# Kernel tuning notes

Measured on AMD Instinct MI355X. Metric: run time of the kernel, lower is better.

## Reference

```python
import jax, jax.numpy as jnp
import numpy as np

B, L, DM, H, DFF = 4, 2048, 512, 8, 2048
D = DM // H            # head dim = 64
FACTOR = 5
U = min(FACTOR * int(np.ceil(np.log(L))), L)  # 40 sampled keys / top-u queries
EPS = 1e-5


def layer_norm(x, g, b):
    m = x.mean(-1, keepdims=True)
    v = ((x - m) ** 2).mean(-1, keepdims=True)
    return (x - m) * jax.lax.rsqrt(v + EPS) * g + b


def setup_inputs() -> dict:
    key = jax.random.key(0)
    ks = jax.random.split(key, 18)
    s = 0.02  # init scale for stability
    return {
        "x": jax.random.normal(ks[0], (B, L, DM), jnp.float32),
        "Wq": jax.random.normal(ks[1], (DM, DM), jnp.float32) * s,
        "bq": jnp.zeros((DM,), jnp.float32),
        "Wk": jax.random.normal(ks[2], (DM, DM), jnp.float32) * s,
        "bk": jnp.zeros((DM,), jnp.float32),
        "Wv": jax.random.normal(ks[3], (DM, DM), jnp.float32) * s,
        "bv": jnp.zeros((DM,), jnp.float32),
        "Wo": jax.random.normal(ks[4], (DM, DM), jnp.float32) * s,
        "bo": jnp.zeros((DM,), jnp.float32),
        "Wc1": jax.random.normal(ks[5], (DFF, DM), jnp.float32) * s,  # conv1d k=1 weight (out,in)
        "bc1": jnp.zeros((DFF,), jnp.float32),
        "Wc2": jax.random.normal(ks[6], (DM, DFF), jnp.float32) * s,
        "bc2": jnp.zeros((DM,), jnp.float32),
        "ln1_g": jnp.ones((DM,), jnp.float32),
        "ln1_b": jnp.zeros((DM,), jnp.float32),
        "ln2_g": jnp.ones((DM,), jnp.float32),
        "ln2_b": jnp.zeros((DM,), jnp.float32),
        "sample_idx": jax.random.randint(ks[7], (L, U), 0, L, jnp.int32),
    }


def reference(x, Wq, bq, Wk, bk, Wv, bv, Wo, bo, Wc1, bc1, Wc2, bc2,
              ln1_g, ln1_b, ln2_g, ln2_b, sample_idx):
    Bb, Ll, _ = x.shape
    # --- AttentionLayer projections -> (B, H, L, D) ---
    q = (x @ Wq + bq).reshape(Bb, Ll, H, D).transpose(0, 2, 1, 3)
    k = (x @ Wk + bk).reshape(Bb, Ll, H, D).transpose(0, 2, 1, 3)
    v = (x @ Wv + bv).reshape(Bb, Ll, H, D).transpose(0, 2, 1, 3)

    # --- ProbSparse: score each query against U sampled keys ---
    K_sample = k[:, :, sample_idx, :]                       # (B,H,L,U,D)
    QK_sample = jnp.einsum('bhld,bhlud->bhlu', q, K_sample)  # (B,H,L,U)
    M = QK_sample.max(-1) - QK_sample.mean(-1)               # sparsity measure (B,H,L)
    _, M_top = jax.lax.top_k(M, U)                           # (B,H,U) top-u query indices

    # --- full attention only for top-u queries ---
    Q_red = jnp.take_along_axis(q, M_top[..., None], axis=2)  # (B,H,U,D)
    scores = jnp.einsum('bhud,bhld->bhul', Q_red, k) / jnp.sqrt(jnp.float32(D))
    attn = jax.nn.softmax(scores, axis=-1)                    # (B,H,U,L)
    ctx_top = jnp.einsum('bhul,bhld->bhud', attn, v)          # (B,H,U,D)

    # --- initial context = mean of V (mask_flag=False); scatter top-u rows ---
    context = jnp.broadcast_to(v.mean(axis=2, keepdims=True), v.shape)
    bi = jnp.arange(Bb)[:, None, None]
    hi = jnp.arange(H)[None, :, None]
    context = context.at[bi, hi, M_top].set(ctx_top)          # (B,H,L,D)

    new_x = context.transpose(0, 2, 1, 3).reshape(Bb, Ll, DM) @ Wo + bo

    # --- residual + norm + conv1d(k=1) FFN + norm ---
    x = layer_norm(x + new_x, ln1_g, ln1_b)
    y = jax.nn.relu(x @ Wc1.T + bc1)
    y = y @ Wc2.T + bc2
    return layer_norm(x + y, ln2_g, ln2_b)
```

## Files before the change

### kernel.cpp

```cpp
#include <hip/hip_runtime.h>
#include <math.h>

static constexpr int Bc = 4, Lc = 2048, DMc = 512, Hc = 8, Dc = 64, DFFc = 2048, Uc = 40;
static constexpr int NT = Bc * Lc;

typedef __attribute__((ext_vector_type(4))) float f32x4;
typedef __attribute__((ext_vector_type(8))) short bf16x8;
typedef unsigned short ushort_t;

__device__ __forceinline__ float wave_sum(float v) {
#pragma unroll
  for (int off = 32; off > 0; off >>= 1) v += __shfl_xor(v, off);
  return v;
}

__device__ __forceinline__ ushort_t f2bf(float f) {
  union { float f; unsigned int u; } c{f};
  unsigned int u = c.u + 0x7fff + ((c.u >> 16) & 1);
  return (ushort_t)(u >> 16);
}

__device__ __forceinline__ float bf2f(ushort_t b) {
  union { unsigned int u; float f; } c{(unsigned int)b << 16};
  return c.f;
}

__device__ __forceinline__ void gload16(const ushort_t* g, ushort_t* l) {
  __builtin_amdgcn_global_load_lds(
      (const __attribute__((address_space(1))) unsigned int*)g,
      (__attribute__((address_space(3))) unsigned int*)l, 16, 0, 0);
}

template <int MODE>
__global__ __launch_bounds__(256) void gemm_mfma(
    const ushort_t* __restrict__ A, const ushort_t* __restrict__ Bt,
    const float* __restrict__ bias, float* __restrict__ Cf,
    ushort_t* __restrict__ Cb, ushort_t* __restrict__ Qo, ushort_t* __restrict__ Ko,
    ushort_t* __restrict__ Vo, int M, int N, int K) {
  __shared__ __align__(16) ushort_t As[128 * 32];
  __shared__ __align__(16) ushort_t Bs[128 * 32];
  const int tid = threadIdx.x;
  const int lane = tid & 63, wave = tid >> 6;
  const int nwg = gridDim.x * gridDim.y;
  const int lin = blockIdx.y * gridDim.x + blockIdx.x;
  const int swz = (lin & 7) * (nwg >> 3) + (lin >> 3);
  const int m0 = (swz / gridDim.x) << 7, n0 = (swz % gridDim.x) << 7;
  const int wm = ((wave >> 1) << 6), wn = ((wave & 1) << 6);
  f32x4 acc[4][4] = {};
  const ushort_t* aSrc = A + (size_t)(m0 + (tid >> 2)) * K + ((tid & 3) << 3);
  const ushort_t* bSrc = Bt + (size_t)(n0 + (tid >> 2)) * K + ((tid & 3) << 3);
  ushort_t* aDst = As + wave * 512;
  ushort_t* bDst = Bs + wave * 512;
  const size_t aHalf = (size_t)64 * K, bHalf = (size_t)64 * K;
  for (int k0 = 0; k0 < K; k0 += 32) {
    gload16(aSrc + k0, aDst);
    gload16(aSrc + aHalf + k0, aDst + 2048);
    gload16(bSrc + k0, bDst);
    gload16(bSrc + bHalf + k0, bDst + 2048);
    __syncthreads();
    bf16x8 af[4], bfr[4];
    const int fr = lane & 15, ko = (lane >> 4) << 3;
#pragma unroll
    for (int i = 0; i < 4; ++i) {
      af[i] = *reinterpret_cast<const bf16x8*>(&As[(wm + i * 16 + fr) * 32 + ko]);
      bfr[i] = *reinterpret_cast<const bf16x8*>(&Bs[(wn + i * 16 + fr) * 32 + ko]);
    }
#pragma unroll
    for (int i = 0; i < 4; ++i)
#pragma unroll
      for (int j = 0; j < 4; ++j)
        acc[i][j] = __builtin_amdgcn_mfma_f32_16x16x32_bf16(af[i], bfr[j], acc[i][j], 0, 0, 0);
    __syncthreads();
  }
  const int cr = (lane >> 4) << 2, cc = lane & 15;
#pragma unroll
  for (int j = 0; j < 4; ++j) {
    const int col = n0 + wn + j * 16 + cc;
    const float bsv = bias[col];
#pragma unroll
    for (int i = 0; i < 4; ++i) {
#pragma unroll
      for (int r = 0; r < 4; ++r) {
        const int row = m0 + wm + i * 16 + cr + r;
        float v = acc[i][j][r] + bsv;
        if (MODE == 0) {
          Cf[(size_t)row * N + col] = v;
        } else if (MODE == 1) {
          Cb[(size_t)row * N + col] = f2bf(fmaxf(v, 0.f));
        } else {
          const int which = col >> 9, h = (col >> 6) & 7, d = col & 63;
          const int b = row >> 11, l = row & (Lc - 1);
          const size_t o = ((size_t)(((b << 3) + h) << 11) + l) * 64 + d;
          ushort_t* dst = which == 0 ? Qo : (which == 1 ? Ko : Vo);
          dst[o] = f2bf(v);
        }
      }
    }
  }
}

__global__ __launch_bounds__(256) void conv_bf16(const float* __restrict__ in,
                                                 ushort_t* __restrict__ out) {
  int i = blockIdx.x * 256 + threadIdx.x;
  float4 v = *reinterpret_cast<const float4*>(&in[(size_t)i * 4]);
  ushort4 o;
  o.x = f2bf(v.x); o.y = f2bf(v.y); o.z = f2bf(v.z); o.w = f2bf(v.w);
  *reinterpret_cast<ushort4*>(&out[(size_t)i * 4]) = o;
}

__global__ __launch_bounds__(256) void tconv(const float* __restrict__ in,
                                             ushort_t* __restrict__ out,
                                             int R, int C, int rowOff) {
  __shared__ float t[32][33];
  const int r0 = blockIdx.y << 5, c0 = blockIdx.x << 5;
  const int tr = threadIdx.x >> 5, tc = threadIdx.x & 31;
#pragma unroll
  for (int p = 0; p < 4; ++p)
    t[tr + p * 8][tc] = in[(size_t)(r0 + tr + p * 8) * C + c0 + tc];
  __syncthreads();
#pragma unroll
  for (int p = 0; p < 4; ++p)
    out[(size_t)(rowOff + c0 + tr + p * 8) * R + r0 + tc] = f2bf(t[tc][tr + p * 8]);
}

__global__ __launch_bounds__(256) void concat_bias(const float* __restrict__ bq,
                                                   const float* __restrict__ bk,
                                                   const float* __restrict__ bv,
                                                   float* __restrict__ o) {
  int i = blockIdx.x * 256 + threadIdx.x;
  o[i] = i < 512 ? bq[i] : (i < 1024 ? bk[i - 512] : bv[i - 1024]);
}

__global__ __launch_bounds__(256) void compute_M_kernel(
    const ushort_t* __restrict__ Q, const ushort_t* __restrict__ K,
    const int* __restrict__ sidx, float* __restrict__ Mout) {
  const int tid = threadIdx.x;
  const int wave = tid >> 6, lane = tid & 63;
  const int g = lane >> 4, lg = lane & 15;
  const int p = blockIdx.x;
  const int xcd = p & 7, j = p >> 3;
  const int bh = xcd + ((j >> 7) << 3);
  const int inner = j & 127;
  const int gw = (bh << 11) + (inner << 4) + wave * 4 + g;
  const int l = gw & (Lc - 1);
  const ushort4 q4 = *reinterpret_cast<const ushort4*>(&Q[((size_t)gw << 6) + (lg << 2)]);
  const float qx = bf2f(q4.x), qy = bf2f(q4.y), qz = bf2f(q4.z), qw = bf2f(q4.w);
  const ushort_t* Kbase = K + ((size_t)bh << 17);
  const int* sp = sidx + l * Uc;
  float mx = -1e30f, sm = 0.f;
#pragma unroll 4
  for (int u = 0; u < Uc; ++u) {
    const int idx = sp[u];
    const ushort4 k4 = *reinterpret_cast<const ushort4*>(&Kbase[((size_t)idx << 6) + (lg << 2)]);
    float d = qx * bf2f(k4.x) + qy * bf2f(k4.y) + qz * bf2f(k4.z) + qw * bf2f(k4.w);
#pragma unroll
    for (int off = 8; off > 0; off >>= 1) d += __shfl_xor(d, off);
    mx = fmaxf(mx, d);
    sm += d;
  }
  if (lg == 0) Mout[gw] = mx - sm * (1.f / Uc);
}

__global__ __launch_bounds__(256) void topk_kernel(const float* __restrict__ Min,
                                                   int* __restrict__ Mtop) {
  __shared__ unsigned sm[Lc];
  __shared__ int scount[4];
  __shared__ int slist[Lc];
  __shared__ int snum;
  const int bh = blockIdx.x;
  const int tid = threadIdx.x;
  const int wv = tid >> 6, lane = tid & 63;
  unsigned sv[8];
#pragma unroll
  for (int t = 0; t < 8; ++t) {
    const unsigned u = __float_as_uint(Min[bh * Lc + tid + (t << 8)]);
    const unsigned s = (u & 0x80000000u) ? ~u : (u | 0x80000000u);
    sv[t] = s;
    sm[tid + (t << 8)] = s;
  }
  if (tid == 0) snum = 0;
  __syncthreads();
  unsigned lo = 0u, hi = 0xFFFFFFFFu;
  while (lo < hi) {
    const unsigned mid =
        (unsigned)(((unsigned long long)lo + (unsigned long long)hi + 1ull) >> 1);
    int cnt = 0;
#pragma unroll
    for (int t = 0; t < 8; ++t) cnt += (sv[t] >= mid);
#pragma unroll
    for (int off = 32; off > 0; off >>= 1) cnt += __shfl_xor(cnt, off);
    if (lane == 0) scount[wv] = cnt;
    __syncthreads();
    const int total = scount[0] + scount[1] + scount[2] + scount[3];
    __syncthreads();
    if (total >= Uc) lo = mid; else hi = mid - 1;
  }
#pragma unroll
  for (int t = 0; t < 8; ++t)
    if (sv[t] >= lo) {
      const int pos = atomicAdd(&snum, 1);
      slist[pos] = tid + (t << 8);
    }
  __syncthreads();
  const int S = snum;
  const int jbase = lane << 5;
  for (int s = wv; s < S; s += 4) {
    const int c = slist[s];
    const unsigned mv = sm[c];
    int rank = 0;
#pragma unroll
    for (int q = 0; q < 8; ++q) {
      const int j = jbase + (q << 2);
      const uint4 w4 = *reinterpret_cast<const uint4*>(&sm[j]);
      rank += (w4.x > mv || (w4.x == mv && (j + 0) < c));
      rank += (w4.y > mv || (w4.y == mv && (j + 1) < c));
      rank += (w4.z > mv || (w4.z == mv && (j + 2) < c));
      rank += (w4.w > mv || (w4.w == mv && (j + 3) < c));
    }
#pragma unroll
    for (int off = 32; off > 0; off >>= 1) rank += __shfl_xor(rank, off);
    if (lane == 0 && rank < Uc) Mtop[bh * Uc + rank] = c;
  }
}

__global__ __launch_bounds__(256, 3) void attn_flash(
    const ushort_t* __restrict__ Q, const ushort_t* __restrict__ K,
    const ushort_t* __restrict__ V, const int* __restrict__ Mtop,
    float* __restrict__ m_p, float* __restrict__ l_p, float* __restrict__ o_p) {
  __shared__ __align__(16) ushort_t Qs[48 * 80];
  __shared__ __align__(16) ushort_t KVs[128 * 80];
  __shared__ __align__(16) ushort_t Ps[48 * 144];
  __shared__ float mw[4][48];
  __shared__ float lw[4][48];
  const int tid = threadIdx.x;
  const int lane = tid & 63, w = tid >> 6;
  const int cc = lane & 15, hi = lane >> 4;
  const int bh = blockIdx.x >> 4, chunk = blockIdx.x & 15;
  const int kk0 = chunk << 7;
  const ushort_t* Qb = Q + ((size_t)bh << 17);
  const ushort_t* Kb = K + ((size_t)bh << 17);
  const ushort_t* Vb = V + ((size_t)bh << 17);

  for (int i = tid; i < 48 * 8; i += 256) {
    const int r = i >> 3, c8 = (i & 7) << 3;
    bf16x8 v = 0;
    if (r < Uc) {
      const int lsel = Mtop[bh * Uc + r];
      v = *reinterpret_cast<const bf16x8*>(&Qb[((size_t)lsel << 6) + c8]);
    }
    *reinterpret_cast<bf16x8*>(&Qs[r * 80 + c8]) = v;
  }
  for (int i = tid; i < 128 * 8; i += 256) {
    const int r = i >> 3, c8 = (i & 7) << 3;
    *reinterpret_cast<bf16x8*>(&KVs[r * 80 + c8]) =
        *reinterpret_cast<const bf16x8*>(&Kb[((size_t)(kk0 + r) << 6) + c8]);
  }
  __syncthreads();

  f32x4 sacc[3][2] = {};
#pragma unroll
  for (int s = 0; s < 2; ++s) {
    bf16x8 af[3], bk[2];
#pragma unroll
    for (int i = 0; i < 3; ++i)
      af[i] = *reinterpret_cast<const bf16x8*>(&Qs[(i * 16 + cc) * 80 + s * 32 + hi * 8]);
#pragma unroll
    for (int jj = 0; jj < 2; ++jj)
      bk[jj] = *reinterpret_cast<const bf16x8*>(&KVs[(w * 32 + jj * 16 + cc) * 80 + s * 32 + hi * 8]);
#pragma unroll
    for (int i = 0; i < 3; ++i)
#pragma unroll
      for (int jj = 0; jj < 2; ++jj)
        sacc[i][jj] = __builtin_amdgcn_mfma_f32_16x16x32_bf16(af[i], bk[jj], sacc[i][jj], 0, 0, 0);
  }

  float mx[3][4];
#pragma unroll
  for (int i = 0; i < 3; ++i)
#pragma unroll
    for (int r = 0; r < 4; ++r)
      mx[i][r] = fmaxf(sacc[i][0][r], sacc[i][1][r]) * 0.125f;
#pragma unroll
  for (int off = 1; off < 16; off <<= 1)
#pragma unroll
    for (int i = 0; i < 3; ++i)
#pragma unroll
      for (int r = 0; r < 4; ++r)
        mx[i][r] = fmaxf(mx[i][r], __shfl_xor(mx[i][r], off));
  if (cc == 0)
#pragma unroll
    for (int i = 0; i < 3; ++i)
#pragma unroll
      for (int r = 0; r < 4; ++r) mw[w][i * 16 + (hi << 2) + r] = mx[i][r];
  __syncthreads();

  float fm[3][4], ls[3][4];
#pragma unroll
  for (int i = 0; i < 3; ++i)
#pragma unroll
    for (int r = 0; r < 4; ++r) {
      const int row = i * 16 + (hi << 2) + r;
      fm[i][r] = fmaxf(fmaxf(mw[0][row], mw[1][row]), fmaxf(mw[2][row], mw[3][row]));
      ls[i][r] = 0.f;
    }
#pragma unroll
  for (int i = 0; i < 3; ++i)
#pragma unroll
    for (int jj = 0; jj < 2; ++jj)
#pragma unroll
      for (int r = 0; r < 4; ++r) {
        float p = __expf(sacc[i][jj][r] * 0.125f - fm[i][r]);
        ls[i][r] += p;
        Ps[(i * 16 + (hi << 2) + r) * 144 + w * 32 + jj * 16 + cc] = f2bf(p);
      }
#pragma unroll
  for (int off = 1; off < 16; off <<= 1)
#pragma unroll
    for (int i = 0; i < 3; ++i)
#pragma unroll
      for (int r = 0; r < 4; ++r) ls[i][r] += __shfl_xor(ls[i][r], off);
  if (cc == 0)
#pragma unroll
    for (int i = 0; i < 3; ++i)
#pragma unroll
      for (int r = 0; r < 4; ++r) lw[w][i * 16 + (hi << 2) + r] = ls[i][r];

  {
    ushort_t* Vt = KVs;
    for (int i = tid; i < 128 * 8; i += 256) {
      const int k = i >> 3, c8 = (i & 7) << 3;
      bf16x8 v = *reinterpret_cast<const bf16x8*>(&Vb[((size_t)(kk0 + k) << 6) + c8]);
#pragma unroll
      for (int jq = 0; jq < 8; ++jq) Vt[(c8 + jq) * 144 + k] = (ushort_t)v[jq];
    }
  }
  __syncthreads();

  f32x4 oacc[3] = {};
#pragma unroll
  for (int s = 0; s < 4; ++s) {
    bf16x8 ap[3], bv;
#pragma unroll
    for (int i = 0; i < 3; ++i)
      ap[i] = *reinterpret_cast<const bf16x8*>(&Ps[(i * 16 + cc) * 144 + s * 32 + hi * 8]);
    bv = *reinterpret_cast<const bf16x8*>(&KVs[(w * 16 + cc) * 144 + s * 32 + hi * 8]);
#pragma unroll
    for (int i = 0; i < 3; ++i)
      oacc[i] = __builtin_amdgcn_mfma_f32_16x16x32_bf16(ap[i], bv, oacc[i], 0, 0, 0);
  }
#pragma unroll
  for (int i = 0; i < 3; ++i)
#pragma unroll
    for (int r = 0; r < 4; ++r) {
      const int row = i * 16 + (hi << 2) + r;
      if (row < Uc)
        o_p[((size_t)((bh * Uc + row) * 16 + chunk) << 6) + w * 16 + cc] = oacc[i][r];
    }
  if (w == 0 && cc == 0)
#pragma unroll
    for (int i = 0; i < 3; ++i)
#pragma unroll
      for (int r = 0; r < 4; ++r) {
        const int row = i * 16 + (hi << 2) + r;
        if (row < Uc) {
          m_p[(bh * Uc + row) * 16 + chunk] = fm[i][r];
          l_p[(bh * Uc + row) * 16 + chunk] =
              lw[0][row] + lw[1][row] + lw[2][row] + lw[3][row];
        }
      }
}

__global__ __launch_bounds__(256) void attn_combine(
    const float* __restrict__ m_p, const float* __restrict__ l_p,
    const float* __restrict__ o_p, const int* __restrict__ Mtop,
    ushort_t* __restrict__ ctxb) {
  const int w = (blockIdx.x * 256 + threadIdx.x) >> 6;
  const int lane = threadIdx.x & 63;
  const float* mp = m_p + w * 16;
  const float* lp = l_p + w * 16;
  float M = -1e30f;
#pragma unroll
  for (int c = 0; c < 16; ++c) M = fmaxf(M, mp[c]);
  float denom = 0.f;
  float wgt[16];
#pragma unroll
  for (int c = 0; c < 16; ++c) {
    wgt[c] = __expf(mp[c] - M);
    denom += lp[c] * wgt[c];
  }
  float acc = 0.f;
#pragma unroll
  for (int c = 0; c < 16; ++c)
    acc += o_p[((size_t)w * 16 + c) * 64 + lane] * wgt[c];
  const int bh = w / Uc;
  const int b = bh >> 3, h = bh & 7;
  const int lsel = Mtop[w];
  ctxb[(size_t)(b * Lc + lsel) * DMc + (h << 6) + lane] = f2bf(acc / denom);
}

__global__ __launch_bounds__(64) void vmean_kernel(const ushort_t* __restrict__ V,
                                                   float* __restrict__ vmean) {
  int blk = blockIdx.x;
  int bh = blk >> 3, c = blk & 7;
  int lane = threadIdx.x;
  float sm = 0.f;
  int lbase = c << 8;
  for (int l = lbase; l < lbase + 256; ++l)
    sm += bf2f(V[((size_t)(bh * Lc + l) << 6) + lane]);
  atomicAdd(&vmean[(bh << 6) + lane], sm * (1.f / Lc));
}

__global__ __launch_bounds__(256) void build_ctx_kernel(const float* __restrict__ vmean,
                                                        ushort_t* __restrict__ ctxb) {
  int idx = blockIdx.x * 256 + threadIdx.x;
  ctxb[idx] = f2bf(vmean[((idx >> 20) << 9) + (idx & 511)]);
}

__global__ __launch_bounds__(256) void add_ln_kernel(
    const float* __restrict__ resid, const float* __restrict__ yin,
    const float* __restrict__ g, const float* __restrict__ bbias,
    float* __restrict__ out, ushort_t* __restrict__ outb) {
  __shared__ float vals[DMc];
  __shared__ float red[4];
  int row = blockIdx.x, tid = threadIdx.x;
  size_t base = (size_t)row * DMc;
  float lsum = 0.f;
  for (int c = tid; c < DMc; c += 256) {
    float t = resid[base + c] + yin[base + c];
    vals[c] = t;
    lsum += t;
  }
  lsum = wave_sum(lsum);
  if ((tid & 63) == 0) red[tid >> 6] = lsum;
  __syncthreads();
  float mean = (red[0] + red[1] + red[2] + red[3]) * (1.f / DMc);
  __syncthreads();
  float lv = 0.f;
  for (int c = tid; c < DMc; c += 256) {
    float dv = vals[c] - mean;
    lv += dv * dv;
  }
  lv = wave_sum(lv);
  if ((tid & 63) == 0) red[tid >> 6] = lv;
  __syncthreads();
  float inv = rsqrtf((red[0] + red[1] + red[2] + red[3]) * (1.f / DMc) + 1e-5f);
  for (int c = tid; c < DMc; c += 256) {
    float o = (vals[c] - mean) * inv * g[c] + bbias[c];
    out[base + c] = o;
    if (outb) outb[base + c] = f2bf(o);
  }
}

extern "C" void kernel_launch(void* const* d_in, const int* in_sizes, int n_in,
                              void* d_out, int out_size, void* d_ws, size_t ws_size,
                              hipStream_t stream) {
  (void)in_sizes; (void)n_in; (void)out_size; (void)ws_size;
  const float* x   = (const float*)d_in[0];
  const float* Wq  = (const float*)d_in[1];
  const float* bq  = (const float*)d_in[2];
  const float* Wk  = (const float*)d_in[3];
  const float* bk  = (const float*)d_in[4];
  const float* Wv  = (const float*)d_in[5];
  const float* bv  = (const float*)d_in[6];
  const float* Wo  = (const float*)d_in[7];
  const float* bo  = (const float*)d_in[8];
  const float* Wc1 = (const float*)d_in[9];
  const float* bc1 = (const float*)d_in[10];
  const float* Wc2 = (const float*)d_in[11];
  const float* bc2 = (const float*)d_in[12];
  const float* g1  = (const float*)d_in[13];
  const float* b1  = (const float*)d_in[14];
  const float* g2  = (const float*)d_in[15];
  const float* b2  = (const float*)d_in[16];
  const int* sidx  = (const int*)d_in[17];
  float* out = (float*)d_out;

  float* ws = (float*)d_ws;
  ushort_t* Qb   = (ushort_t*)ws;
  ushort_t* Kb   = (ushort_t*)(ws + 4194304);
  ushort_t* Vb   = (ushort_t*)(ws + 8388608);
  float* m_p    = ws + 12582912;
  float* l_p    = ws + 12603392;
  float* o_p    = ws + 12623872;
  float* X1     = ws + 16777216;
  ushort_t* xb   = (ushort_t*)(ws + 20971520);
  ushort_t* Wqkvt= (ushort_t*)(ws + 23068672);
  ushort_t* Wot  = (ushort_t*)(ws + 23461888);
  ushort_t* Wc1b = (ushort_t*)(ws + 23592960);
  ushort_t* Wc2b = (ushort_t*)(ws + 24117248);
  float* bqkv   = ws + 24641536;
  float* Mb     = ws + 24643072;
  float* vmean  = ws + 24708608;
  int* Mtop     = (int*)(ws + 24710656);
  ushort_t* CTXb = Vb;
  ushort_t* X1b  = (ushort_t*)(ws + 12582912);
  ushort_t* Yb   = (ushort_t*)ws;

  dim3 blk(256);
  conv_bf16<<<4096, blk, 0, stream>>>(x, xb);
  tconv<<<dim3(16, 16), blk, 0, stream>>>(Wq, Wqkvt, 512, 512, 0);
  tconv<<<dim3(16, 16), blk, 0, stream>>>(Wk, Wqkvt, 512, 512, 512);
  tconv<<<dim3(16, 16), blk, 0, stream>>>(Wv, Wqkvt, 512, 512, 1024);
  tconv<<<dim3(16, 16), blk, 0, stream>>>(Wo, Wot, 512, 512, 0);
  conv_bf16<<<1024, blk, 0, stream>>>(Wc1, Wc1b);
  conv_bf16<<<1024, blk, 0, stream>>>(Wc2, Wc2b);
  concat_bias<<<6, blk, 0, stream>>>(bq, bk, bv, bqkv);

  gemm_mfma<2><<<dim3(12, 64), blk, 0, stream>>>(xb, Wqkvt, bqkv, nullptr, nullptr,
                                                 Qb, Kb, Vb, NT, 1536, DMc);
  compute_M_kernel<<<4096, blk, 0, stream>>>(Qb, Kb, sidx, Mb);
  topk_kernel<<<32, blk, 0, stream>>>(Mb, Mtop);
  attn_flash<<<512, blk, 0, stream>>>(Qb, Kb, Vb, Mtop, m_p, l_p, o_p);
  hipMemsetAsync(vmean, 0, Bc * Hc * Dc * sizeof(float), stream);
  vmean_kernel<<<Bc * Hc * 8, dim3(64), 0, stream>>>(Vb, vmean);
  build_ctx_kernel<<<16384, blk, 0, stream>>>(vmean, CTXb);
  attn_combine<<<320, blk, 0, stream>>>(m_p, l_p, o_p, Mtop, CTXb);

  gemm_mfma<0><<<dim3(4, 64), blk, 0, stream>>>(CTXb, Wot, bo, out, nullptr,
                                                nullptr, nullptr, nullptr,
                                                NT, DMc, DMc);
  add_ln_kernel<<<NT, blk, 0, stream>>>(x, out, g1, b1, X1, X1b);
  gemm_mfma<1><<<dim3(16, 64), blk, 0, stream>>>(X1b, Wc1b, bc1, nullptr, Yb,
                                                 nullptr, nullptr, nullptr,
                                                 NT, DFFc, DMc);
  gemm_mfma<0><<<dim3(4, 64), blk, 0, stream>>>(Yb, Wc2b, bc2, out, nullptr,
                                                nullptr, nullptr, nullptr,
                                                NT, DMc, DFFc);
  add_ln_kernel<<<NT, blk, 0, stream>>>(X1, out, g2, b2, out, nullptr);
}
```

Baseline: 356.8 us.

## Split-K the N=512 GEMMs and fuse weight-prep launches into one kernel

The two output-width-512 GEMMs (Wo projection and second FFN conv) are run as split-K with two halves of K. Each half writes its own fp32 partial buffer, and the following add+LayerNorm kernel sums both partials, so grid occupancy doubles from 256 to 512 workgroups. The eight small conversion, transpose and bias-concat launches are merged into a single prep kernel to cut launch overhead. The cost is an extra fp32 partial write and read, plus reuse of workspace regions for the partials, which must not overlap any buffer still live.

```diff
diff --git a/kernel.cpp b/kernel.cpp
--- a/kernel.cpp
+++ b/kernel.cpp
@@ -35,8 +35,9 @@
 __global__ __launch_bounds__(256) void gemm_mfma(
     const ushort_t* __restrict__ A, const ushort_t* __restrict__ Bt,
     const float* __restrict__ bias, float* __restrict__ Cf,
-    ushort_t* __restrict__ Cb, ushort_t* __restrict__ Qo, ushort_t* __restrict__ Ko,
-    ushort_t* __restrict__ Vo, int M, int N, int K) {
+    float* __restrict__ Cf1, ushort_t* __restrict__ Cb,
+    ushort_t* __restrict__ Qo, ushort_t* __restrict__ Ko,
+    ushort_t* __restrict__ Vo, int M, int N, int K, int Kh) {
   __shared__ __align__(16) ushort_t As[128 * 32];
   __shared__ __align__(16) ushort_t Bs[128 * 32];
   const int tid = threadIdx.x;
@@ -44,15 +45,25 @@
   const int nwg = gridDim.x * gridDim.y;
   const int lin = blockIdx.y * gridDim.x + blockIdx.x;
   const int swz = (lin & 7) * (nwg >> 3) + (lin >> 3);
-  const int m0 = (swz / gridDim.x) << 7, n0 = (swz % gridDim.x) << 7;
+  int m0, n0, kpart = 0;
+  if (MODE == 3) {
+    const int gy = swz / gridDim.x;
+    n0 = (swz % gridDim.x) << 7;
+    m0 = (gy & 63) << 7;
+    kpart = gy >> 6;
+  } else {
+    m0 = (swz / gridDim.x) << 7;
+    n0 = (swz % gridDim.x) << 7;
+  }
+  const int kOff = kpart * Kh;
   const int wm = ((wave >> 1) << 6), wn = ((wave & 1) << 6);
   f32x4 acc[4][4] = {};
-  const ushort_t* aSrc = A + (size_t)(m0 + (tid >> 2)) * K + ((tid & 3) << 3);
-  const ushort_t* bSrc = Bt + (size_t)(n0 + (tid >> 2)) * K + ((tid & 3) << 3);
+  const ushort_t* aSrc = A + (size_t)(m0 + (tid >> 2)) * K + ((tid & 3) << 3) + kOff;
+  const ushort_t* bSrc = Bt + (size_t)(n0 + (tid >> 2)) * K + ((tid & 3) << 3) + kOff;
   ushort_t* aDst = As + wave * 512;
   ushort_t* bDst = Bs + wave * 512;
   const size_t aHalf = (size_t)64 * K, bHalf = (size_t)64 * K;
-  for (int k0 = 0; k0 < K; k0 += 32) {
+  for (int k0 = 0; k0 < Kh; k0 += 32) {
     gload16(aSrc + k0, aDst);
     gload16(aSrc + aHalf + k0, aDst + 2048);
     gload16(bSrc + k0, bDst);
@@ -82,12 +93,16 @@
 #pragma unroll
       for (int r = 0; r < 4; ++r) {
         const int row = m0 + wm + i * 16 + cr + r;
-        float v = acc[i][j][r] + bsv;
+        float v = acc[i][j][r];
         if (MODE == 0) {
-          Cf[(size_t)row * N + col] = v;
+          Cf[(size_t)row * N + col] = v + bsv;
         } else if (MODE == 1) {
-          Cb[(size_t)row * N + col] = f2bf(fmaxf(v, 0.f));
+          Cb[(size_t)row * N + col] = f2bf(fmaxf(v + bsv, 0.f));
+        } else if (MODE == 3) {
+          float* dstf = kpart ? Cf1 : Cf;
+          dstf[(size_t)row * N + col] = kpart ? v : v + bsv;
         } else {
+          v += bsv;
           const int which = col >> 9, h = (col >> 6) & 7, d = col & 63;
           const int b = row >> 11, l = row & (Lc - 1);
           const size_t o = ((size_t)(((b << 3) + h) << 11) + l) * 64 + d;
@@ -99,36 +114,50 @@
   }
 }
 
-__global__ __launch_bounds__(256) void conv_bf16(const float* __restrict__ in,
-                                                 ushort_t* __restrict__ out) {
-  int i = blockIdx.x * 256 + threadIdx.x;
-  float4 v = *reinterpret_cast<const float4*>(&in[(size_t)i * 4]);
-  ushort4 o;
-  o.x = f2bf(v.x); o.y = f2bf(v.y); o.z = f2bf(v.z); o.w = f2bf(v.w);
-  *reinterpret_cast<ushort4*>(&out[(size_t)i * 4]) = o;
-}
-
-__global__ __launch_bounds__(256) void tconv(const float* __restrict__ in,
-                                             ushort_t* __restrict__ out,
-                                             int R, int C, int rowOff) {
+__global__ __launch_bounds__(256) void prep_kernel(
+    const float* __restrict__ x, const float* __restrict__ Wq,
+    const float* __restrict__ Wk, const float* __restrict__ Wv,
+    const float* __restrict__ Wo, const float* __restrict__ Wc1,
+    const float* __restrict__ Wc2, const float* __restrict__ bq,
+    const float* __restrict__ bk, const float* __restrict__ bv,
+    ushort_t* __restrict__ xb, ushort_t* __restrict__ Wqkvt,
+    ushort_t* __restrict__ Wot, ushort_t* __restrict__ Wc1b,
+    ushort_t* __restrict__ Wc2b, float* __restrict__ bqkv) {
   __shared__ float t[32][33];
-  const int r0 = blockIdx.y << 5, c0 = blockIdx.x << 5;
-  const int tr = threadIdx.x >> 5, tc = threadIdx.x & 31;
-#pragma unroll
-  for (int p = 0; p < 4; ++p)
-    t[tr + p * 8][tc] = in[(size_t)(r0 + tr + p * 8) * C + c0 + tc];
-  __syncthreads();
-#pragma unroll
-  for (int p = 0; p < 4; ++p)
-    out[(size_t)(rowOff + c0 + tr + p * 8) * R + r0 + tc] = f2bf(t[tc][tr + p * 8]);
-}
-
-__global__ __launch_bounds__(256) void concat_bias(const float* __restrict__ bq,
-                                                   const float* __restrict__ bk,
-                                                   const float* __restrict__ bv,
-                                                   float* __restrict__ o) {
-  int i = blockIdx.x * 256 + threadIdx.x;
-  o[i] = i < 512 ? bq[i] : (i < 1024 ? bk[i - 512] : bv[i - 1024]);
+  const int blk = blockIdx.x, tid = threadIdx.x;
+  if (blk < 4096) {
+    const int i = blk * 256 + tid;
+    float4 v = *reinterpret_cast<const float4*>(&x[(size_t)i * 4]);
+    ushort4 o;
+    o.x = f2bf(v.x); o.y = f2bf(v.y); o.z = f2bf(v.z); o.w = f2bf(v.w);
+    *reinterpret_cast<ushort4*>(&xb[(size_t)i * 4]) = o;
+  } else if (blk < 5120) {
+    const int wsel = (blk - 4096) >> 8, tt = (blk - 4096) & 255;
+    const float* src = wsel == 0 ? Wq : (wsel == 1 ? Wk : (wsel == 2 ? Wv : Wo));
+    ushort_t* dst = wsel == 3 ? Wot : Wqkvt;
+    const int rowOff = wsel == 1 ? 512 : (wsel == 2 ? 1024 : 0);
+    const int r0 = (tt >> 4) << 5, c0 = (tt & 15) << 5;
+    const int tr = tid >> 5, tc = tid & 31;
+#pragma unroll
+    for (int p = 0; p < 4; ++p)
+      t[tr + p * 8][tc] = src[(size_t)(r0 + tr + p * 8) * 512 + c0 + tc];
+    __syncthreads();
+#pragma unroll
+    for (int p = 0; p < 4; ++p)
+      dst[(size_t)(rowOff + c0 + tr + p * 8) * 512 + r0 + tc] = f2bf(t[tc][tr + p * 8]);
+  } else if (blk < 7168) {
+    const int which = (blk - 5120) >> 10;
+    const int i = ((blk - 5120) & 1023) * 256 + tid;
+    const float* src = which == 0 ? Wc1 : Wc2;
+    ushort_t* dst = which == 0 ? Wc1b : Wc2b;
+    float4 v = *reinterpret_cast<const float4*>(&src[(size_t)i * 4]);
+    ushort4 o;
+    o.x = f2bf(v.x); o.y = f2bf(v.y); o.z = f2bf(v.z); o.w = f2bf(v.w);
+    *reinterpret_cast<ushort4*>(&dst[(size_t)i * 4]) = o;
+  } else {
+    const int i = (blk - 7168) * 256 + tid;
+    bqkv[i] = i < 512 ? bq[i] : (i < 1024 ? bk[i - 512] : bv[i - 1024]);
+  }
 }
 
 __global__ __launch_bounds__(256) void compute_M_kernel(
@@ -418,8 +447,9 @@
 
 __global__ __launch_bounds__(256) void add_ln_kernel(
     const float* __restrict__ resid, const float* __restrict__ yin,
-    const float* __restrict__ g, const float* __restrict__ bbias,
-    float* __restrict__ out, ushort_t* __restrict__ outb) {
+    const float* __restrict__ yin2, const float* __restrict__ g,
+    const float* __restrict__ bbias, float* __restrict__ out,
+    ushort_t* __restrict__ outb) {
   __shared__ float vals[DMc];
   __shared__ float red[4];
   int row = blockIdx.x, tid = threadIdx.x;
@@ -427,6 +457,7 @@
   float lsum = 0.f;
   for (int c = tid; c < DMc; c += 256) {
     float t = resid[base + c] + yin[base + c];
+    if (yin2) t += yin2[base + c];
     vals[c] = t;
     lsum += t;
   }
@@ -495,19 +526,15 @@
   ushort_t* CTXb = Vb;
   ushort_t* X1b  = (ushort_t*)(ws + 12582912);
   ushort_t* Yb   = (ushort_t*)ws;
+  float* woP1   = ws + 4194304;
+  float* ffP1   = ws + 8388608;
 
   dim3 blk(256);
-  conv_bf16<<<4096, blk, 0, stream>>>(x, xb);
-  tconv<<<dim3(16, 16), blk, 0, stream>>>(Wq, Wqkvt, 512, 512, 0);
-  tconv<<<dim3(16, 16), blk, 0, stream>>>(Wk, Wqkvt, 512, 512, 512);
-  tconv<<<dim3(16, 16), blk, 0, stream>>>(Wv, Wqkvt, 512, 512, 1024);
-  tconv<<<dim3(16, 16), blk, 0, stream>>>(Wo, Wot, 512, 512, 0);
-  conv_bf16<<<1024, blk, 0, stream>>>(Wc1, Wc1b);
-  conv_bf16<<<1024, blk, 0, stream>>>(Wc2, Wc2b);
-  concat_bias<<<6, blk, 0, stream>>>(bq, bk, bv, bqkv);
+  prep_kernel<<<7174, blk, 0, stream>>>(x, Wq, Wk, Wv, Wo, Wc1, Wc2, bq, bk, bv,
+                                        xb, Wqkvt, Wot, Wc1b, Wc2b, bqkv);
 
   gemm_mfma<2><<<dim3(12, 64), blk, 0, stream>>>(xb, Wqkvt, bqkv, nullptr, nullptr,
-                                                 Qb, Kb, Vb, NT, 1536, DMc);
+                                                 nullptr, Qb, Kb, Vb, NT, 1536, DMc, DMc);
   compute_M_kernel<<<4096, blk, 0, stream>>>(Qb, Kb, sidx, Mb);
   topk_kernel<<<32, blk, 0, stream>>>(Mb, Mtop);
   attn_flash<<<512, blk, 0, stream>>>(Qb, Kb, Vb, Mtop, m_p, l_p, o_p);
@@ -516,15 +543,15 @@
   build_ctx_kernel<<<16384, blk, 0, stream>>>(vmean, CTXb);
   attn_combine<<<320, blk, 0, stream>>>(m_p, l_p, o_p, Mtop, CTXb);
 
-  gemm_mfma<0><<<dim3(4, 64), blk, 0, stream>>>(CTXb, Wot, bo, out, nullptr,
-                                                nullptr, nullptr, nullptr,
-                                                NT, DMc, DMc);
-  add_ln_kernel<<<NT, blk, 0, stream>>>(x, out, g1, b1, X1, X1b);
-  gemm_mfma<1><<<dim3(16, 64), blk, 0, stream>>>(X1b, Wc1b, bc1, nullptr, Yb,
-                                                 nullptr, nullptr, nullptr,
-                                                 NT, DFFc, DMc);
-  gemm_mfma<0><<<dim3(4, 64), blk, 0, stream>>>(Yb, Wc2b, bc2, out, nullptr,
-                                                nullptr, nullptr, nullptr,
-                                                NT, DMc, DFFc);
-  add_ln_kernel<<<NT, blk, 0, stream>>>(X1, out, g2, b2, out, nullptr);
-}
+  gemm_mfma<3><<<dim3(4, 128), blk, 0, stream>>>(CTXb, Wot, bo, out, woP1,
+                                                 nullptr, nullptr, nullptr, nullptr,
+                                                 NT, DMc, DMc, DMc / 2);
+  add_ln_kernel<<<NT, blk, 0, stream>>>(x, out, woP1, g1, b1, X1, X1b);
+  gemm_mfma<1><<<dim3(16, 64), blk, 0, stream>>>(X1b, Wc1b, bc1, nullptr, nullptr,
+                                                 Yb, nullptr, nullptr, nullptr,
+                                                 NT, DFFc, DMc, DMc);
+  gemm_mfma<3><<<dim3(4, 128), blk, 0, stream>>>(Yb, Wc2b, bc2, out, ffP1,
+                                                 nullptr, nullptr, nullptr, nullptr,
+                                                 NT, DMc, DFFc, DFFc / 2);
+  add_ln_kernel<<<NT, blk, 0, stream>>>(X1, out, ffP1, g2, b2, out, nullptr);
+}
```

Result: faster. 327.7 us (-8.1%).
